# Kernel tuning notes

Measured on AMD Instinct MI355X. Metric: run time of the kernel, lower is better.

The kernel has to match this reference:

```python
import jax, jax.numpy as jnp
import numpy as np

HIDDEN = 1024
NUM_GAUSS = 20
BATCH = 512
SEQ = 1024
VOCAB = 128


def setup_inputs() -> dict:
    key = jax.random.key(0)
    k1, k2, k3, k4 = jax.random.split(key, 4)
    window_input = jax.random.normal(k1, (BATCH, HIDDEN), dtype=jnp.float32)
    sentence_hot = jax.random.uniform(k2, (BATCH, SEQ, VOCAB), dtype=jnp.float32)
    kappa_prev = jnp.zeros((BATCH, NUM_GAUSS), dtype=jnp.float32)
    # Linear(hidden_size -> 3*num_gauss_conv); small init so exp() stays bounded
    W = jax.random.normal(k3, (3 * NUM_GAUSS, HIDDEN), dtype=jnp.float32) * 0.02
    b = jax.random.normal(k4, (3 * NUM_GAUSS,), dtype=jnp.float32) * 0.02
    return {"window_input": window_input, "sentence_hot": sentence_hot,
            "kappa_prev": kappa_prev, "W": W, "b": b}


def reference(window_input, sentence_hot, kappa_prev, W, b):
    K = NUM_GAUSS
    # linear layer: [B, 3K]
    lin = window_input @ W.T + b
    alpha = jnp.exp(lin[:, :K])                       # [B, K]
    beta = jnp.exp(lin[:, K:2 * K])                   # [B, K]
    kappa = kappa_prev + jnp.exp(lin[:, 2 * K:]) * 0.05  # [B, K]
    U = sentence_hot.shape[1]
    u = jnp.arange(U, dtype=lin.dtype)                # [U]
    # phi_k: [B, K, U] = alpha * exp(-beta * (kappa - u)^2)
    diff = kappa[:, :, None] - u[None, None, :]
    phi_k = alpha[:, :, None] * jnp.exp(-beta[:, :, None] * diff * diff)
    phi = jnp.sum(phi_k, axis=1)[:, :, None]          # [B, U, 1]
    # wind: [B, vocab] = sum_u phi[b,u] * sentence_hot[b,u,v]
    wind = jnp.einsum('bu,buv->bv', phi[:, :, 0], sentence_hot)
    return (wind, kappa, phi)
```

## Files before the change

### kernel.cpp

```cpp
#include <hip/hip_runtime.h>

#define HIDDEN 1024
#define NG 20
#define BATCH 512
#define SEQ 1024
#define VOCAB 128

#define WIND_OFF  0
#define KAPPA_OFF (BATCH * VOCAB)
#define PHI_OFF   (BATCH * VOCAB + BATCH * NG)

typedef float f4 __attribute__((ext_vector_type(4)));

__global__ __launch_bounds__(256) void gates_phi(
    const float* __restrict__ win,
    const float* __restrict__ kprev,
    const float* __restrict__ W,
    const float* __restrict__ bias,
    float*       __restrict__ out)
{
    const int b    = blockIdx.x;
    const int tid  = threadIdx.x;
    const int lane = tid & 63;
    const int wave = tid >> 6;

    __shared__ float lin_s[3 * NG];
    __shared__ float alpha_s[NG], beta_s[NG], kappa_s[NG];

    if (tid < VOCAB) out[WIND_OFF + (size_t)b * VOCAB + tid] = 0.f;

    const float* wrow = win + (size_t)b * HIDDEN;
    for (int j = wave; j < 3 * NG; j += 4) {
        const float* Wrow = W + (size_t)j * HIDDEN;
        float acc = 0.f;
        #pragma unroll
        for (int t = 0; t < HIDDEN / 64; ++t)
            acc = fmaf(wrow[t * 64 + lane], Wrow[t * 64 + lane], acc);
        #pragma unroll
        for (int off = 32; off > 0; off >>= 1)
            acc += __shfl_down(acc, off, 64);
        if (lane == 0) lin_s[j] = acc + bias[j];
    }
    __syncthreads();

    if (tid < 3 * NG) {
        float e = __expf(lin_s[tid]);
        if (tid < NG) {
            alpha_s[tid] = e;
        } else if (tid < 2 * NG) {
            beta_s[tid - NG] = e;
        } else {
            int k = tid - 2 * NG;
            float kp = kprev[(size_t)b * NG + k] + e * 0.05f;
            kappa_s[k] = kp;
            out[KAPPA_OFF + (size_t)b * NG + k] = kp;
        }
    }
    __syncthreads();

    for (int u = tid; u < SEQ; u += 256) {
        float uu = (float)u;
        float p = 0.f;
        #pragma unroll
        for (int k = 0; k < NG; ++k) {
            float d = kappa_s[k] - uu;
            p = fmaf(alpha_s[k], __expf(-beta_s[k] * d * d), p);
        }
        out[PHI_OFF + (size_t)b * SEQ + u] = p;
    }
}

__global__ __launch_bounds__(256) void wind_einsum(
    const f4*    __restrict__ sh4,
    const float* __restrict__ phi,
    float*       __restrict__ wind)
{
    const int b   = blockIdx.x >> 2;
    const int uc  = blockIdx.x & 3;
    const int tid = threadIdx.x;

    __shared__ float phi_s[256];
    __shared__ float red[8][VOCAB];

    phi_s[tid] = phi[(size_t)b * SEQ + uc * 256 + tid];
    __syncthreads();

    const int vq = tid & 31;
    const int ug = tid >> 5;
    const f4* base = sh4 + ((size_t)b * SEQ + uc * 256) * (VOCAB / 4);

    f4 acc = (f4){0.f, 0.f, 0.f, 0.f};
    #pragma unroll 8
    for (int i = 0; i < 32; ++i) {
        int u = ug + 8 * i;
        f4 s = __builtin_nontemporal_load(base + (size_t)u * (VOCAB / 4) + vq);
        acc += phi_s[u] * s;
    }
    *(f4*)&red[ug][vq * 4] = acc;
    __syncthreads();

    if (tid < VOCAB) {
        float s = 0.f;
        #pragma unroll
        for (int g = 0; g < 8; ++g) s += red[g][tid];
        atomicAdd(&wind[(size_t)b * VOCAB + tid], s);
    }
}

extern "C" void kernel_launch(void* const* d_in, const int* in_sizes, int n_in,
                              void* d_out, int out_size, void* d_ws, size_t ws_size,
                              hipStream_t stream) {
    const float* win   = (const float*)d_in[0];
    const f4*    sh4   = (const f4*)d_in[1];
    const float* kprev = (const float*)d_in[2];
    const float* W     = (const float*)d_in[3];
    const float* bias  = (const float*)d_in[4];
    float* out = (float*)d_out;

    gates_phi<<<dim3(BATCH), dim3(256), 0, stream>>>(win, kprev, W, bias, out);
    wind_einsum<<<dim3(BATCH * 4), dim3(256), 0, stream>>>(
        sh4, out + PHI_OFF, out + WIND_OFF);
}
```

Measured before the change: 356.0 us.

## Move phi computation into wind kernel and vectorize gate dot products

The first kernel now only computes alpha/beta/kappa, writing them to workspace. The second kernel computes its 256-element phi slice directly into shared memory, so it no longer reads phi back from global memory, and the phi work is spread over four times as many blocks. The gate dot products now use float4 loads. The cost is an extra small workspace round trip. The dominant cost, streaming the 256MB sentence tensor, is unchanged.

```diff
diff --git a/kernel.cpp b/kernel.cpp
--- a/kernel.cpp
+++ b/kernel.cpp
@@ -12,12 +12,17 @@
 
 typedef float f4 __attribute__((ext_vector_type(4)));
 
-__global__ __launch_bounds__(256) void gates_phi(
-    const float* __restrict__ win,
+#define WS_ALPHA 0
+#define WS_BETA  (BATCH * NG)
+#define WS_KAPPA (2 * BATCH * NG)
+
+__global__ __launch_bounds__(256) void gates_k(
+    const f4*    __restrict__ win4,
     const float* __restrict__ kprev,
-    const float* __restrict__ W,
+    const f4*    __restrict__ W4,
     const float* __restrict__ bias,
-    float*       __restrict__ out)
+    float*       __restrict__ out,
+    float*       __restrict__ ws)
 {
     const int b    = blockIdx.x;
     const int tid  = threadIdx.x;
@@ -25,17 +30,22 @@
     const int wave = tid >> 6;
 
     __shared__ float lin_s[3 * NG];
-    __shared__ float alpha_s[NG], beta_s[NG], kappa_s[NG];
 
     if (tid < VOCAB) out[WIND_OFF + (size_t)b * VOCAB + tid] = 0.f;
 
-    const float* wrow = win + (size_t)b * HIDDEN;
+    const f4* wrow = win4 + (size_t)b * (HIDDEN / 4);
     for (int j = wave; j < 3 * NG; j += 4) {
-        const float* Wrow = W + (size_t)j * HIDDEN;
+        const f4* Wrow = W4 + (size_t)j * (HIDDEN / 4);
         float acc = 0.f;
         #pragma unroll
-        for (int t = 0; t < HIDDEN / 64; ++t)
-            acc = fmaf(wrow[t * 64 + lane], Wrow[t * 64 + lane], acc);
+        for (int t = 0; t < HIDDEN / 4 / 64; ++t) {
+            f4 a = wrow[t * 64 + lane];
+            f4 w = Wrow[t * 64 + lane];
+            acc = fmaf(a.x, w.x, acc);
+            acc = fmaf(a.y, w.y, acc);
+            acc = fmaf(a.z, w.z, acc);
+            acc = fmaf(a.w, w.w, acc);
+        }
         #pragma unroll
         for (int off = 32; off > 0; off >>= 1)
             acc += __shfl_down(acc, off, 64);
@@ -46,43 +56,47 @@
     if (tid < 3 * NG) {
         float e = __expf(lin_s[tid]);
         if (tid < NG) {
-            alpha_s[tid] = e;
+            ws[WS_ALPHA + (size_t)b * NG + tid] = e;
         } else if (tid < 2 * NG) {
-            beta_s[tid - NG] = e;
+            ws[WS_BETA + (size_t)b * NG + (tid - NG)] = e;
         } else {
             int k = tid - 2 * NG;
             float kp = kprev[(size_t)b * NG + k] + e * 0.05f;
-            kappa_s[k] = kp;
+            ws[WS_KAPPA + (size_t)b * NG + k] = kp;
             out[KAPPA_OFF + (size_t)b * NG + k] = kp;
         }
     }
+}
+
+__global__ __launch_bounds__(256) void phi_wind_k(
+    const f4*    __restrict__ sh4,
+    const float* __restrict__ ws,
+    float*       __restrict__ out)
+{
+    const int b   = blockIdx.x >> 2;
+    const int uc  = blockIdx.x & 3;
+    const int tid = threadIdx.x;
+
+    __shared__ float alpha_s[NG], beta_s[NG], kappa_s[NG];
+    __shared__ float phi_s[256];
+    __shared__ float red[8][VOCAB];
+
+    if (tid < NG)                 alpha_s[tid]          = ws[WS_ALPHA + (size_t)b * NG + tid];
+    else if (tid < 2 * NG)        beta_s[tid - NG]      = ws[WS_BETA  + (size_t)b * NG + (tid - NG)];
+    else if (tid < 3 * NG)        kappa_s[tid - 2 * NG] = ws[WS_KAPPA + (size_t)b * NG + (tid - 2 * NG)];
     __syncthreads();
 
-    for (int u = tid; u < SEQ; u += 256) {
-        float uu = (float)u;
+    {
+        const float uu = (float)(uc * 256 + tid);
         float p = 0.f;
         #pragma unroll
         for (int k = 0; k < NG; ++k) {
             float d = kappa_s[k] - uu;
             p = fmaf(alpha_s[k], __expf(-beta_s[k] * d * d), p);
         }
-        out[PHI_OFF + (size_t)b * SEQ + u] = p;
+        phi_s[tid] = p;
+        out[PHI_OFF + (size_t)b * SEQ + uc * 256 + tid] = p;
     }
-}
-
-__global__ __launch_bounds__(256) void wind_einsum(
-    const f4*    __restrict__ sh4,
-    const float* __restrict__ phi,
-    float*       __restrict__ wind)
-{
-    const int b   = blockIdx.x >> 2;
-    const int uc  = blockIdx.x & 3;
-    const int tid = threadIdx.x;
-
-    __shared__ float phi_s[256];
-    __shared__ float red[8][VOCAB];
-
-    phi_s[tid] = phi[(size_t)b * SEQ + uc * 256 + tid];
     __syncthreads();
 
     const int vq = tid & 31;
@@ -103,21 +117,21 @@
         float s = 0.f;
         #pragma unroll
         for (int g = 0; g < 8; ++g) s += red[g][tid];
-        atomicAdd(&wind[(size_t)b * VOCAB + tid], s);
+        atomicAdd(&out[WIND_OFF + (size_t)b * VOCAB + tid], s);
     }
 }
 
 extern "C" void kernel_launch(void* const* d_in, const int* in_sizes, int n_in,
                               void* d_out, int out_size, void* d_ws, size_t ws_size,
                               hipStream_t stream) {
-    const float* win   = (const float*)d_in[0];
+    const f4*    win4  = (const f4*)d_in[0];
     const f4*    sh4   = (const f4*)d_in[1];
     const float* kprev = (const float*)d_in[2];
-    const float* W     = (const float*)d_in[3];
+    const f4*    W4    = (const f4*)d_in[3];
     const float* bias  = (const float*)d_in[4];
     float* out = (float*)d_out;
+    float* ws  = (float*)d_ws;
 
-    gates_phi<<<dim3(BATCH), dim3(256), 0, stream>>>(win, kprev, W, bias, out);
-    wind_einsum<<<dim3(BATCH * 4), dim3(256), 0, stream>>>(
-        sh4, out + PHI_OFF, out + WIND_OFF);
+    gates_k<<<dim3(BATCH), dim3(256), 0, stream>>>(win4, kprev, W4, bias, out, ws);
+    phi_wind_k<<<dim3(BATCH * 4), dim3(256), 0, stream>>>(sh4, ws, out);
 }
```

Measured after the change: 354.0 us. About the same (-0.6%).
